# Kernel optimization log

Measured on AMD Instinct MI355X. Metric: run time of the kernel, lower is better.

Reference implementation:

```python
import jax, jax.numpy as jnp
import numpy as np

N_QUBITS = 3
N_LAYERS = 2
EPS = 1e-12  # torch F.normalize eps


def _apply_1q(state, U, q):
    # state: (B, 2, 2, 2) complex, qubit q on axis q+1 (wire 0 = MSB, PennyLane convention)
    ax = q + 1
    s = jnp.moveaxis(state, ax, -1)
    s = jnp.einsum('...j,ij->...i', s, U)
    return jnp.moveaxis(s, -1, ax)


def _apply_cnot(state, c, t):
    # flip target qubit t where control qubit c is |1>
    ca, ta = c + 1, t + 1
    s0 = jnp.take(state, 0, axis=ca)
    s1 = jnp.take(state, 1, axis=ca)
    flip_ax = ta if ta < ca else ta - 1  # axis index after removing ca
    s1 = jnp.flip(s1, axis=flip_ax)
    return jnp.stack([s0, s1], axis=ca)


def _ry(theta):
    c, s = jnp.cos(theta / 2), jnp.sin(theta / 2)
    return jnp.array([[c, -s], [s, c]]).astype(jnp.complex64)


def _rz(theta):
    return jnp.array([[jnp.exp(-1j * theta / 2), 0.0 + 0.0j],
                      [0.0 + 0.0j, jnp.exp(1j * theta / 2)]]).astype(jnp.complex64)


def setup_inputs() -> dict:
    key = jax.random.key(0)
    k1, k2, k3, k4 = jax.random.split(key, 4)
    B, F, V = 262144, 512, 8
    x = jax.random.normal(k1, (B, F), dtype=jnp.float32)
    # nn.Linear(512, 8): kaiming-uniform-ish init
    bound = 1.0 / np.sqrt(F)
    W_proj = jax.random.uniform(k2, (V, F), minval=-bound, maxval=bound, dtype=jnp.float32)
    b_proj = jax.random.uniform(k3, (V,), minval=-bound, maxval=bound, dtype=jnp.float32)
    # TorchLayer default init: uniform in [0, 2pi); shape (n_layers, 2, n_qubits)
    vqc_weights = jax.random.uniform(k4, (N_LAYERS, 2, N_QUBITS), minval=0.0,
                                     maxval=2 * np.pi, dtype=jnp.float32)
    return {"x": x, "W_proj": W_proj, "b_proj": b_proj, "vqc_weights": vqc_weights}


def reference(x, W_proj, b_proj, vqc_weights):
    B = x.shape[0]
    projected = jnp.tanh(x @ W_proj.T + b_proj)                       # (B, 8)
    norm = jnp.linalg.norm(projected, axis=1, keepdims=True)
    projected_norm = projected / jnp.maximum(norm, EPS)               # (B, 8), unit L2
    # AmplitudeEmbedding(normalize=True): state amplitudes = normalized vector
    state = projected_norm.astype(jnp.complex64).reshape(B, 2, 2, 2)  # wire0 = MSB
    for l in range(N_LAYERS):
        for q in range(N_QUBITS):
            state = _apply_1q(state, _ry(vqc_weights[l, 0, q]), q)
        for q in range(N_QUBITS):
            state = _apply_1q(state, _rz(vqc_weights[l, 1, q]), q)
        for q in range(N_QUBITS - 1):
            state = _apply_cnot(state, q, q + 1)
        state = _apply_cnot(state, N_QUBITS - 1, 0)
    probs = state.real ** 2 + state.imag ** 2                         # (B, 2, 2, 2)
    z = []
    for q in range(N_QUBITS):
        p = jnp.moveaxis(probs, q + 1, 1).reshape(B, 2, -1)
        z.append(p[:, 0].sum(-1) - p[:, 1].sum(-1))                   # <Z_q>
    quantum_out = jnp.stack(z, axis=1)                                # (B, 3)
    return jnp.concatenate([projected, quantum_out], axis=1)          # (B, 11)
```

## Files before the change

### kernel.cpp

```cpp
#include <hip/hip_runtime.h>
#include <math.h>

__global__ __launch_bounds__(64) void vqc_build_u(const float* __restrict__ wq,
                                                  float* __restrict__ Uws) {
  const int j = threadIdx.x;
  if (j >= 8) return;
  float ar[8], ai[8];
#pragma unroll
  for (int i = 0; i < 8; ++i) { ar[i] = (i == j) ? 1.f : 0.f; ai[i] = 0.f; }

#pragma unroll
  for (int l = 0; l < 2; ++l) {
#pragma unroll
    for (int q = 0; q < 3; ++q) {
      const float th = 0.5f * wq[l * 6 + q];
      const float c = cosf(th), s = sinf(th);
      const int bit = 4 >> q;
#pragma unroll
      for (int i0 = 0; i0 < 8; ++i0) {
        if (i0 & bit) continue;
        const int i1 = i0 | bit;
        const float r0 = ar[i0], m0 = ai[i0], r1 = ar[i1], m1 = ai[i1];
        ar[i0] = c * r0 - s * r1;  ai[i0] = c * m0 - s * m1;
        ar[i1] = s * r0 + c * r1;  ai[i1] = s * m0 + c * m1;
      }
    }
#pragma unroll
    for (int q = 0; q < 3; ++q) {
      const float th = 0.5f * wq[l * 6 + 3 + q];
      const float c = cosf(th), s = sinf(th);
      const int bit = 4 >> q;
#pragma unroll
      for (int i = 0; i < 8; ++i) {
        const float r = ar[i], m = ai[i];
        if (i & bit) { ar[i] = r * c - m * s;  ai[i] = m * c + r * s; }
        else         { ar[i] = r * c + m * s;  ai[i] = m * c - r * s; }
      }
    }
#pragma unroll
    for (int k = 0; k < 3; ++k) {
      const int cb = (k == 0) ? 4 : (k == 1) ? 2 : 1;
      const int tb = (k == 0) ? 2 : (k == 1) ? 1 : 4;
#pragma unroll
      for (int i = 0; i < 8; ++i) {
        if ((i & cb) && !(i & tb)) {
          const int i1 = i | tb;
          float t;
          t = ar[i]; ar[i] = ar[i1]; ar[i1] = t;
          t = ai[i]; ai[i] = ai[i1]; ai[i1] = t;
        }
      }
    }
  }
#pragma unroll
  for (int i = 0; i < 8; ++i) {
    Uws[i * 8 + j]      = ar[i];
    Uws[64 + i * 8 + j] = ai[i];
  }
}

__global__ __launch_bounds__(256, 4) void vqc_fused(const float* __restrict__ x,
                                                    const float* __restrict__ W,
                                                    const float* __restrict__ bias,
                                                    const float* __restrict__ Uws,
                                                    float* __restrict__ out, int B) {
  const int lane = threadIdx.x & 63;
  const int wid  = blockIdx.x * (blockDim.x >> 6) + (threadIdx.x >> 6);
  const int nw   = gridDim.x * (blockDim.x >> 6);
  const bool b0 = (lane & 1) != 0;
  const bool b1 = (lane & 2) != 0;
  const bool b2 = (lane & 4) != 0;
  const int grp = lane >> 3;
  const int myv = ((lane & 1) << 2) | (lane & 2) | ((lane >> 2) & 1);

  float w0[8][4], w1[8][4];
#pragma unroll
  for (int v = 0; v < 8; ++v) {
    const float4 a = *(const float4*)(W + v * 512 + lane * 4);
    const float4 b = *(const float4*)(W + v * 512 + 256 + lane * 4);
    w0[v][0] = a.x; w0[v][1] = a.y; w0[v][2] = a.z; w0[v][3] = a.w;
    w1[v][0] = b.x; w1[v][1] = b.y; w1[v][2] = b.z; w1[v][3] = b.w;
  }
  float Ur[8], Ui[8];
#pragma unroll
  for (int i = 0; i < 8; ++i) {
    Ur[i] = Uws[i * 8 + myv];
    Ui[i] = Uws[64 + i * 8 + myv];
  }
  const float bv = bias[myv];

  const int nbatch = (B + 7) >> 3;
  for (int rb = wid; rb < nbatch; rb += nw) {
    const int r0 = rb << 3;
    float myd = 0.f;
#pragma unroll
    for (int t = 0; t < 8; ++t) {
      const int r = r0 + t;
      if (r < B) {
        const float4* xr = (const float4*)(x + (size_t)r * 512);
        const float4 xa = xr[lane];
        const float4 xb = xr[64 + lane];
        float acc[8];
#pragma unroll
        for (int v = 0; v < 8; ++v) {
          float s = xa.x * w0[v][0];
          s = fmaf(xa.y, w0[v][1], s);
          s = fmaf(xa.z, w0[v][2], s);
          s = fmaf(xa.w, w0[v][3], s);
          s = fmaf(xb.x, w1[v][0], s);
          s = fmaf(xb.y, w1[v][1], s);
          s = fmaf(xb.z, w1[v][2], s);
          s = fmaf(xb.w, w1[v][3], s);
          acc[v] = s;
        }
        float s4[4];
#pragma unroll
        for (int i = 0; i < 4; ++i) {
          const float keep = b0 ? acc[i + 4] : acc[i];
          const float send = b0 ? acc[i] : acc[i + 4];
          s4[i] = keep + __shfl_xor(send, 1, 64);
        }
        float s2[2];
#pragma unroll
        for (int i = 0; i < 2; ++i) {
          const float keep = b1 ? s4[i + 2] : s4[i];
          const float send = b1 ? s4[i] : s4[i + 2];
          s2[i] = keep + __shfl_xor(send, 2, 64);
        }
        const float keep = b2 ? s2[1] : s2[0];
        const float send = b2 ? s2[0] : s2[1];
        float s1 = keep + __shfl_xor(send, 4, 64);
        s1 += __shfl_xor(s1, 8, 64);
        s1 += __shfl_xor(s1, 16, 64);
        s1 += __shfl_xor(s1, 32, 64);
        myd = (grp == t) ? s1 : myd;
      }
    }

    const int row = r0 + grp;
    const float p = tanhf(myd + bv);
    float ss = p * p;
    ss += __shfl_xor(ss, 1, 64);
    ss += __shfl_xor(ss, 2, 64);
    ss += __shfl_xor(ss, 4, 64);
    const float av = p * (1.0f / fmaxf(sqrtf(ss), 1e-12f));

    float q[16];
#pragma unroll
    for (int i = 0; i < 8; ++i) {
      q[2 * i]     = Ur[i] * av;
      q[2 * i + 1] = Ui[i] * av;
    }
    float n8[8];
#pragma unroll
    for (int i = 0; i < 8; ++i) {
      const float k1 = b0 ? q[i + 8] : q[i];
      const float s1v = b0 ? q[i] : q[i + 8];
      n8[i] = k1 + __shfl_xor(s1v, 1, 64);
    }
    float n4[4];
#pragma unroll
    for (int i = 0; i < 4; ++i) {
      const float k2 = b1 ? n8[i + 4] : n8[i];
      const float s2v = b1 ? n8[i] : n8[i + 4];
      n4[i] = k2 + __shfl_xor(s2v, 2, 64);
    }
    float n2[2];
#pragma unroll
    for (int i = 0; i < 2; ++i) {
      const float k3 = b2 ? n4[i + 2] : n4[i];
      const float s3v = b2 ? n4[i] : n4[i + 2];
      n2[i] = k3 + __shfl_xor(s3v, 4, 64);
    }
    const float pr = n2[0] * n2[0] + n2[1] * n2[1];
    float t0 = (myv & 4) ? -pr : pr;
    float t1 = (myv & 2) ? -pr : pr;
    float t2 = (myv & 1) ? -pr : pr;
#pragma unroll
    for (int m = 1; m <= 4; m <<= 1) {
      t0 += __shfl_xor(t0, m, 64);
      t1 += __shfl_xor(t1, m, 64);
      t2 += __shfl_xor(t2, m, 64);
    }
    if (row < B) {
      float* o = out + (size_t)row * 11;
      o[myv] = p;
      if (myv < 3) o[8 + myv] = (myv == 0) ? t0 : ((myv == 1) ? t1 : t2);
    }
  }
}

extern "C" void kernel_launch(void* const* d_in, const int* in_sizes, int n_in,
                              void* d_out, int out_size, void* d_ws, size_t ws_size,
                              hipStream_t stream) {
  const float* x  = (const float*)d_in[0];
  const float* W  = (const float*)d_in[1];
  const float* b  = (const float*)d_in[2];
  const float* wq = (const float*)d_in[3];
  float* out = (float*)d_out;
  float* Uws = (float*)d_ws;

  const int B = in_sizes[0] / 512;

  vqc_build_u<<<1, 64, 0, stream>>>(wq, Uws);
  vqc_fused<<<2048, 256, 0, stream>>>(x, W, b, Uws, out, B);
}
```

Measured before the change: 115.0 us.

## Batch-load all eight rows before compute and template out bounds checks

Each wave now issues all sixteen float4 loads for its eight rows before any FMA work, rather than interleaving one row's load with its reduction. The goal is more memory-level parallelism on a bandwidth-bound 512 MB read. A template parameter removes the per-row bounds checks when B is a multiple of 8, and launch bounds are relaxed from 4 to 2 blocks per SIMD so the extra 64 live registers fit. Lower occupancy could hurt latency hiding if the compiler spills or if fewer waves in flight outweighs the gain from wider per-wave loads.

```diff
diff --git a/kernel.cpp b/kernel.cpp
--- a/kernel.cpp
+++ b/kernel.cpp
@@ -59,7 +59,8 @@
   }
 }
 
-__global__ __launch_bounds__(256, 4) void vqc_fused(const float* __restrict__ x,
+template<bool GUARD>
+__global__ __launch_bounds__(256, 2) void vqc_fused(const float* __restrict__ x,
                                                     const float* __restrict__ W,
                                                     const float* __restrict__ bias,
                                                     const float* __restrict__ Uws,
@@ -91,53 +92,58 @@
 
   const int nbatch = (B + 7) >> 3;
   for (int rb = wid; rb < nbatch; rb += nw) {
-    const int r0 = rb << 3;
+    const size_t r0 = (size_t)rb << 3;
+
+    float4 xa[8], xb[8];
+#pragma unroll
+    for (int t = 0; t < 8; ++t) {
+      size_t r = r0 + t;
+      if (GUARD) r = (r < (size_t)B) ? r : (size_t)(B - 1);
+      const float4* xr = (const float4*)(x + r * 512);
+      xa[t] = xr[lane];
+      xb[t] = xr[64 + lane];
+    }
+
     float myd = 0.f;
 #pragma unroll
     for (int t = 0; t < 8; ++t) {
-      const int r = r0 + t;
-      if (r < B) {
-        const float4* xr = (const float4*)(x + (size_t)r * 512);
-        const float4 xa = xr[lane];
-        const float4 xb = xr[64 + lane];
-        float acc[8];
-#pragma unroll
-        for (int v = 0; v < 8; ++v) {
-          float s = xa.x * w0[v][0];
-          s = fmaf(xa.y, w0[v][1], s);
-          s = fmaf(xa.z, w0[v][2], s);
-          s = fmaf(xa.w, w0[v][3], s);
-          s = fmaf(xb.x, w1[v][0], s);
-          s = fmaf(xb.y, w1[v][1], s);
-          s = fmaf(xb.z, w1[v][2], s);
-          s = fmaf(xb.w, w1[v][3], s);
-          acc[v] = s;
-        }
-        float s4[4];
-#pragma unroll
-        for (int i = 0; i < 4; ++i) {
-          const float keep = b0 ? acc[i + 4] : acc[i];
-          const float send = b0 ? acc[i] : acc[i + 4];
-          s4[i] = keep + __shfl_xor(send, 1, 64);
-        }
-        float s2[2];
-#pragma unroll
-        for (int i = 0; i < 2; ++i) {
-          const float keep = b1 ? s4[i + 2] : s4[i];
-          const float send = b1 ? s4[i] : s4[i + 2];
-          s2[i] = keep + __shfl_xor(send, 2, 64);
-        }
-        const float keep = b2 ? s2[1] : s2[0];
-        const float send = b2 ? s2[0] : s2[1];
-        float s1 = keep + __shfl_xor(send, 4, 64);
-        s1 += __shfl_xor(s1, 8, 64);
-        s1 += __shfl_xor(s1, 16, 64);
-        s1 += __shfl_xor(s1, 32, 64);
-        myd = (grp == t) ? s1 : myd;
-      }
-    }
-
-    const int row = r0 + grp;
+      float acc[8];
+#pragma unroll
+      for (int v = 0; v < 8; ++v) {
+        float s = xa[t].x * w0[v][0];
+        s = fmaf(xa[t].y, w0[v][1], s);
+        s = fmaf(xa[t].z, w0[v][2], s);
+        s = fmaf(xa[t].w, w0[v][3], s);
+        s = fmaf(xb[t].x, w1[v][0], s);
+        s = fmaf(xb[t].y, w1[v][1], s);
+        s = fmaf(xb[t].z, w1[v][2], s);
+        s = fmaf(xb[t].w, w1[v][3], s);
+        acc[v] = s;
+      }
+      float s4[4];
+#pragma unroll
+      for (int i = 0; i < 4; ++i) {
+        const float keep = b0 ? acc[i + 4] : acc[i];
+        const float send = b0 ? acc[i] : acc[i + 4];
+        s4[i] = keep + __shfl_xor(send, 1, 64);
+      }
+      float s2[2];
+#pragma unroll
+      for (int i = 0; i < 2; ++i) {
+        const float keep = b1 ? s4[i + 2] : s4[i];
+        const float send = b1 ? s4[i] : s4[i + 2];
+        s2[i] = keep + __shfl_xor(send, 2, 64);
+      }
+      const float keep = b2 ? s2[1] : s2[0];
+      const float send = b2 ? s2[0] : s2[1];
+      float s1 = keep + __shfl_xor(send, 4, 64);
+      s1 += __shfl_xor(s1, 8, 64);
+      s1 += __shfl_xor(s1, 16, 64);
+      s1 += __shfl_xor(s1, 32, 64);
+      myd = (grp == t) ? s1 : myd;
+    }
+
+    const size_t row = r0 + grp;
     const float p = tanhf(myd + bv);
     float ss = p * p;
     ss += __shfl_xor(ss, 1, 64);
@@ -182,8 +188,8 @@
       t1 += __shfl_xor(t1, m, 64);
       t2 += __shfl_xor(t2, m, 64);
     }
-    if (row < B) {
-      float* o = out + (size_t)row * 11;
+    if (!GUARD || row < (size_t)B) {
+      float* o = out + row * 11;
       o[myv] = p;
       if (myv < 3) o[8 + myv] = (myv == 0) ? t0 : ((myv == 1) ? t1 : t2);
     }
@@ -203,5 +209,8 @@
   const int B = in_sizes[0] / 512;
 
   vqc_build_u<<<1, 64, 0, stream>>>(wq, Uws);
-  vqc_fused<<<2048, 256, 0, stream>>>(x, W, b, Uws, out, B);
+  if (B & 7)
+    vqc_fused<true><<<2048, 256, 0, stream>>>(x, W, b, Uws, out, B);
+  else
+    vqc_fused<false><<<2048, 256, 0, stream>>>(x, W, b, Uws, out, B);
 }
```

Measured after the change: 114.9 us. About the same (-0.1%).
